# Performance work log

Measured on AMD Instinct MI355X. Metric: run time of the kernel, lower is better.

The kernel has to match this reference:

```python
import jax, jax.numpy as jnp
import numpy as np

N_NODES = 100000


def _gcn_norm(edge_index, num_nodes):
    # add self loops
    src, dst = edge_index[0], edge_index[1]
    loop = jnp.arange(num_nodes, dtype=src.dtype)
    row = jnp.concatenate([src, loop])  # [E+N]
    col = jnp.concatenate([dst, loop])
    ew = jnp.ones(row.shape[0], dtype=jnp.float32)
    deg = jax.ops.segment_sum(ew, col, num_segments=num_nodes)  # [N]
    dinv = jnp.where(deg > 0, jax.lax.rsqrt(deg), 0.0)
    norm = dinv[row] * ew * dinv[col]  # [E+N]
    return row, col, norm


def setup_inputs() -> dict:
    key = jax.random.key(0)
    k1, k2, k3 = jax.random.split(key, 3)
    x = jax.random.normal(k1, (N_NODES, 64), dtype=jnp.float32)
    edge_index = jax.random.randint(k2, (2, 1280000), 0, N_NODES, dtype=jnp.int64)
    W = jax.random.normal(k3, (40, 64), dtype=jnp.float32) * (1.0 / np.sqrt(64))
    b = jnp.zeros((40,), dtype=jnp.float32)
    return {"x": x, "edge_index": edge_index, "W": W, "b": b}


def reference(x, edge_index, W, b):
    K = 3
    row, col, norm = _gcn_norm(edge_index, N_NODES)
    h = x
    for _ in range(K):
        # gather from source nodes, scale by symmetric norm, scatter-add to dst
        msg = norm[:, None] * h[row]  # [E+N, F]
        h = jax.ops.segment_sum(msg, col, num_segments=N_NODES)
    logits = h @ W.T + b  # [N, C]
    return jax.nn.log_softmax(logits, axis=1)
```

## Files before the change

kernel.cpp:

```cpp
#include <hip/hip_runtime.h>

#define F_IN 64
#define F_OUT 40
#define USTRIDE 32
#define UQ4 8
#define QPN 5

#define PART_BLK 256
#define PART_EPB 16
#define PART_TILE (PART_BLK * PART_EPB)
#define BSHIFT 8
#define BCAP 4096
#define MAXB 512

#define WSTRIDE 17
#define NPB 51

__device__ inline unsigned pk2(float x, float y) {
    unsigned a = __float_as_uint(x); a = (a + 0x7FFFu + ((a >> 16) & 1u)) >> 16;
    unsigned b = __float_as_uint(y); b = (b + 0x7FFFu + ((b >> 16) & 1u)) >> 16;
    return a | (b << 16);
}
__device__ inline void up2(unsigned u, float& a, float& b) {
    a = __uint_as_float(u << 16); b = __uint_as_float(u & 0xFFFF0000u);
}

__global__ __launch_bounds__(PART_BLK) void partition_kernel(const int* __restrict__ src,
                                                             const int* __restrict__ dst,
                                                             int* __restrict__ bfill,
                                                             unsigned* __restrict__ staging,
                                                             int E, int nbk) {
    __shared__ int hist[MAXB];
    __shared__ int base[MAXB];
    int tid = threadIdx.x;
    for (int b = tid; b < nbk; b += PART_BLK) hist[b] = 0;
    __syncthreads();

    int rank[PART_EPB];
    int bk[PART_EPB];
    unsigned rec[PART_EPB];
    int eb = blockIdx.x * PART_TILE + tid;
#pragma unroll
    for (int k = 0; k < PART_EPB; ++k) {
        int e = eb + k * PART_BLK;
        if (e < E) {
            int r = src[e];
            int c = dst[e];
            int b = c >> BSHIFT;
            bk[k] = b;
            rec[k] = (unsigned)r | ((unsigned)(c & 255) << 17);
            rank[k] = atomicAdd(&hist[b], 1);
        } else {
            bk[k] = -1;
        }
    }
    __syncthreads();
    for (int b = tid; b < nbk; b += PART_BLK) {
        int h = hist[b];
        base[b] = h ? (b * BCAP + atomicAdd(&bfill[b], h)) : 0;
    }
    __syncthreads();
#pragma unroll
    for (int k = 0; k < PART_EPB; ++k) {
        if (bk[k] >= 0) staging[base[bk[k]] + rank[k]] = rec[k];
    }
}

__global__ __launch_bounds__(256) void bucket_finalize_kernel(const unsigned* __restrict__ staging,
                                                              const int* __restrict__ bfill,
                                                              int* __restrict__ rowptr,
                                                              float* __restrict__ dinv,
                                                              float* __restrict__ dinv2,
                                                              int* __restrict__ srcs, int n, int E) {
    int b = blockIdx.x;
    __shared__ int h[256];
    __shared__ int cur[256];
    __shared__ int sbase;
    int tid = threadIdx.x;
    h[tid] = 0;
    if (tid == 0) sbase = 0;
    __syncthreads();

    int part = 0;
    for (int j = tid; j < b; j += 256) part += bfill[j];
    if (part) atomicAdd(&sbase, part);

    int cnt = bfill[b];
    const unsigned* rec = staging + (size_t)b * BCAP;
    for (int i = tid; i < cnt; i += 256) {
        atomicAdd(&h[rec[i] >> 17], 1);
    }
    __syncthreads();

    int base = sbase;
    int v = h[tid];
    for (int off = 1; off < 256; off <<= 1) {
        int t = (tid >= off) ? h[tid - off] : 0;
        __syncthreads();
        h[tid] += t;
        __syncthreads();
    }
    int excl = h[tid] - v;
    int node = (b << BSHIFT) | tid;
    if (node < n) {
        rowptr[node] = base + excl;
        float r = rsqrtf((float)v + 1.0f);
        dinv[node] = r;
        dinv2[node] = r * r;
    }
    if (b == 0 && tid == 0) rowptr[n] = E;
    cur[tid] = base + excl;
    __syncthreads();

    for (int i = tid; i < cnt; i += 256) {
        unsigned rv = rec[i];
        int pos = atomicAdd(&cur[rv >> 17], 1);
        srcs[pos] = (int)(rv & 0x1FFFFu);
    }
}

__global__ __launch_bounds__(256, 4) void proj_kernel(const float* __restrict__ x,
                                                      const float* __restrict__ W,
                                                      const float* __restrict__ dinv,
                                                      unsigned* __restrict__ u, int n) {
    __shared__ float Ws[F_OUT * WSTRIDE * 4];
    for (int i = threadIdx.x; i < F_OUT * F_IN; i += 256) {
        int c = i >> 6;
        int k = i & 63;
        Ws[c * (WSTRIDE * 4) + k] = W[i];
    }
    __syncthreads();

    int t = blockIdx.x * 256 + threadIdx.x;
    int g = t >> 2;
    int q = t & 3;
    int n0 = 2 * g;
    if (n0 >= n) return;
    int n1 = n0 + 1;

    const float4* xp0 = (const float4*)(x + (size_t)n0 * F_IN);
    const float4* xp1 = (const float4*)(x + (size_t)n1 * F_IN);
    const float4* Wq  = (const float4*)Ws + (size_t)(q * 10) * WSTRIDE;

    float acc0[10], acc1[10];
#pragma unroll
    for (int c = 0; c < 10; ++c) { acc0[c] = 0.0f; acc1[c] = 0.0f; }

#pragma unroll 1
    for (int f4 = 0; f4 < F_IN / 4; ++f4) {
        float4 x0 = xp0[f4];
        float4 x1 = xp1[f4];
#pragma unroll
        for (int c = 0; c < 10; ++c) {
            float4 w = Wq[c * WSTRIDE + f4];
            acc0[c] += x0.x * w.x + x0.y * w.y + x0.z * w.z + x0.w * w.w;
            acc1[c] += x1.x * w.x + x1.y * w.y + x1.z * w.z + x1.w * w.w;
        }
    }

    float d0 = dinv[n0];
    float d1 = dinv[n1];
    unsigned* up0 = u + (size_t)n0 * USTRIDE + q * 5;
    unsigned* up1 = u + (size_t)n1 * USTRIDE + q * 5;
#pragma unroll
    for (int j = 0; j < 5; ++j) {
        up0[j] = pk2(d0 * acc0[2 * j], d0 * acc0[2 * j + 1]);
        up1[j] = pk2(d1 * acc1[2 * j], d1 * acc1[2 * j + 1]);
    }
}

__global__ __launch_bounds__(256) void propagate_kernel(const int* __restrict__ rowptr,
                                                        const int* __restrict__ srcs,
                                                        const float* __restrict__ dinv2,
                                                        const unsigned* __restrict__ ucur,
                                                        unsigned* __restrict__ unew, int n) {
    int t = blockIdx.x * blockDim.x + threadIdx.x;
    int node = t / QPN;
    int q = t - node * QPN;
    if (node >= n) return;

    int beg = rowptr[node];
    int end = rowptr[node + 1];

    const uint4* U = (const uint4*)ucur;
    uint4 sv = U[(size_t)node * UQ4 + q];
    float a0, a1, a2, a3, a4, a5, a6, a7;
    up2(sv.x, a0, a1); up2(sv.y, a2, a3); up2(sv.z, a4, a5); up2(sv.w, a6, a7);

    int i = beg;
    for (; i + 3 < end; i += 4) {
        int s0 = srcs[i], s1 = srcs[i + 1], s2 = srcs[i + 2], s3 = srcs[i + 3];
        uint4 v0 = U[(size_t)s0 * UQ4 + q];
        uint4 v1 = U[(size_t)s1 * UQ4 + q];
        uint4 v2 = U[(size_t)s2 * UQ4 + q];
        uint4 v3 = U[(size_t)s3 * UQ4 + q];
        float b0, b1;
        up2(v0.x, b0, b1); a0 += b0; a1 += b1;
        up2(v0.y, b0, b1); a2 += b0; a3 += b1;
        up2(v0.z, b0, b1); a4 += b0; a5 += b1;
        up2(v0.w, b0, b1); a6 += b0; a7 += b1;
        up2(v1.x, b0, b1); a0 += b0; a1 += b1;
        up2(v1.y, b0, b1); a2 += b0; a3 += b1;
        up2(v1.z, b0, b1); a4 += b0; a5 += b1;
        up2(v1.w, b0, b1); a6 += b0; a7 += b1;
        up2(v2.x, b0, b1); a0 += b0; a1 += b1;
        up2(v2.y, b0, b1); a2 += b0; a3 += b1;
        up2(v2.z, b0, b1); a4 += b0; a5 += b1;
        up2(v2.w, b0, b1); a6 += b0; a7 += b1;
        up2(v3.x, b0, b1); a0 += b0; a1 += b1;
        up2(v3.y, b0, b1); a2 += b0; a3 += b1;
        up2(v3.z, b0, b1); a4 += b0; a5 += b1;
        up2(v3.w, b0, b1); a6 += b0; a7 += b1;
    }
    for (; i < end; ++i) {
        uint4 v = U[(size_t)srcs[i] * UQ4 + q];
        float b0, b1;
        up2(v.x, b0, b1); a0 += b0; a1 += b1;
        up2(v.y, b0, b1); a2 += b0; a3 += b1;
        up2(v.z, b0, b1); a4 += b0; a5 += b1;
        up2(v.w, b0, b1); a6 += b0; a7 += b1;
    }

    float ds = dinv2[node];
    uint4 o;
    o.x = pk2(ds * a0, ds * a1);
    o.y = pk2(ds * a2, ds * a3);
    o.z = pk2(ds * a4, ds * a5);
    o.w = pk2(ds * a6, ds * a7);
    ((uint4*)unew)[(size_t)node * UQ4 + q] = o;
}

__global__ __launch_bounds__(256) void propagate_lsm_kernel(const int* __restrict__ rowptr,
                                                            const int* __restrict__ srcs,
                                                            const float* __restrict__ dinv,
                                                            const unsigned* __restrict__ ucur,
                                                            const float* __restrict__ bias,
                                                            float* __restrict__ out, int n) {
    __shared__ float red[256];
    int tid = threadIdx.x;
    int gl = tid / QPN;
    int q  = tid - gl * QPN;
    int node = blockIdx.x * NPB + gl;
    bool active = (gl < NPB) && (node < n);

    float a0 = 0, a1 = 0, a2 = 0, a3 = 0, a4 = 0, a5 = 0, a6 = 0, a7 = 0;
    float dv = 0.0f;
    if (active) {
        int beg = rowptr[node];
        int end = rowptr[node + 1];
        const uint4* U = (const uint4*)ucur;
        uint4 sv = U[(size_t)node * UQ4 + q];
        up2(sv.x, a0, a1); up2(sv.y, a2, a3); up2(sv.z, a4, a5); up2(sv.w, a6, a7);
        int i = beg;
        for (; i + 3 < end; i += 4) {
            int s0 = srcs[i], s1 = srcs[i + 1], s2 = srcs[i + 2], s3 = srcs[i + 3];
            uint4 v0 = U[(size_t)s0 * UQ4 + q];
            uint4 v1 = U[(size_t)s1 * UQ4 + q];
            uint4 v2 = U[(size_t)s2 * UQ4 + q];
            uint4 v3 = U[(size_t)s3 * UQ4 + q];
            float b0, b1;
            up2(v0.x, b0, b1); a0 += b0; a1 += b1;
            up2(v0.y, b0, b1); a2 += b0; a3 += b1;
            up2(v0.z, b0, b1); a4 += b0; a5 += b1;
            up2(v0.w, b0, b1); a6 += b0; a7 += b1;
            up2(v1.x, b0, b1); a0 += b0; a1 += b1;
            up2(v1.y, b0, b1); a2 += b0; a3 += b1;
            up2(v1.z, b0, b1); a4 += b0; a5 += b1;
            up2(v1.w, b0, b1); a6 += b0; a7 += b1;
            up2(v2.x, b0, b1); a0 += b0; a1 += b1;
            up2(v2.y, b0, b1); a2 += b0; a3 += b1;
            up2(v2.z, b0, b1); a4 += b0; a5 += b1;
            up2(v2.w, b0, b1); a6 += b0; a7 += b1;
            up2(v3.x, b0, b1); a0 += b0; a1 += b1;
            up2(v3.y, b0, b1); a2 += b0; a3 += b1;
            up2(v3.z, b0, b1); a4 += b0; a5 += b1;
            up2(v3.w, b0, b1); a6 += b0; a7 += b1;
        }
        for (; i < end; ++i) {
            uint4 v = U[(size_t)srcs[i] * UQ4 + q];
            float b0, b1;
            up2(v.x, b0, b1); a0 += b0; a1 += b1;
            up2(v.y, b0, b1); a2 += b0; a3 += b1;
            up2(v.z, b0, b1); a4 += b0; a5 += b1;
            up2(v.w, b0, b1); a6 += b0; a7 += b1;
        }
        dv = dinv[node];
    }

    float y0 = dv * a0 + bias[q * 8 + 0];
    float y1 = dv * a1 + bias[q * 8 + 1];
    float y2 = dv * a2 + bias[q * 8 + 2];
    float y3 = dv * a3 + bias[q * 8 + 3];
    float y4 = dv * a4 + bias[q * 8 + 4];
    float y5 = dv * a5 + bias[q * 8 + 5];
    float y6 = dv * a6 + bias[q * 8 + 6];
    float y7 = dv * a7 + bias[q * 8 + 7];

    float pm = fmaxf(fmaxf(fmaxf(y0, y1), fmaxf(y2, y3)),
                     fmaxf(fmaxf(y4, y5), fmaxf(y6, y7)));
    red[tid] = active ? pm : -1e30f;
    __syncthreads();
    int base = tid - q;
    float mx = fmaxf(fmaxf(fmaxf(red[base], red[base + 1]), fmaxf(red[base + 2], red[base + 3])),
                     red[base + 4]);
    __syncthreads();
    float ps = __expf(y0 - mx) + __expf(y1 - mx) + __expf(y2 - mx) + __expf(y3 - mx)
             + __expf(y4 - mx) + __expf(y5 - mx) + __expf(y6 - mx) + __expf(y7 - mx);
    red[tid] = active ? ps : 0.0f;
    __syncthreads();
    float se = red[base] + red[base + 1] + red[base + 2] + red[base + 3] + red[base + 4];
    float lse = mx + __logf(se);

    if (active) {
        float4* p = (float4*)(out + (size_t)node * F_OUT + q * 8);
        float4 o0, o1;
        o0.x = y0 - lse; o0.y = y1 - lse; o0.z = y2 - lse; o0.w = y3 - lse;
        o1.x = y4 - lse; o1.y = y5 - lse; o1.z = y6 - lse; o1.w = y7 - lse;
        p[0] = o0;
        p[1] = o1;
    }
}

extern "C" void kernel_launch(void* const* d_in, const int* in_sizes, int n_in,
                              void* d_out, int out_size, void* d_ws, size_t ws_size,
                              hipStream_t stream) {
    const float* x  = (const float*)d_in[0];
    const int*   ei = (const int*)d_in[1];
    const float* W  = (const float*)d_in[2];
    const float* b  = (const float*)d_in[3];

    const int N = in_sizes[0] / F_IN;
    const int E = in_sizes[1] / 2;
    const int* src = ei;
    const int* dst = ei + E;
    const int nbk = (N + (1 << BSHIFT) - 1) >> BSHIFT;

    char* base = (char*)d_ws;
    size_t off = 0;
    auto alloc = [&](size_t bytes) {
        char* p = base + off;
        off = (off + bytes + 255) & ~(size_t)255;
        return p;
    };
    float*    dinv    = (float*)   alloc((size_t)N * 4);
    float*    dinv2   = (float*)   alloc((size_t)N * 4);
    int*      rowptr  = (int*)     alloc((size_t)(N + 1) * 4);
    int*      bfill   = (int*)     alloc((size_t)MAXB * 4);
    unsigned* staging = (unsigned*)alloc((size_t)nbk * BCAP * 4);
    int*      srcs_s  = (int*)     alloc((size_t)E * 4);
    unsigned* uA      = (unsigned*)alloc((size_t)N * USTRIDE * 4);
    unsigned* uB      = (unsigned*)alloc((size_t)N * USTRIDE * 4);
    float*    outp    = (float*)d_out;

    hipMemsetAsync(bfill, 0, (size_t)nbk * 4, stream);
    partition_kernel<<<(E + PART_TILE - 1) / PART_TILE, PART_BLK, 0, stream>>>(
        src, dst, bfill, staging, E, nbk);

    bucket_finalize_kernel<<<nbk, 256, 0, stream>>>(staging, bfill, rowptr,
                                                    dinv, dinv2, srcs_s, N, E);

    proj_kernel<<<((size_t)N * 2 + 255) / 256, 256, 0, stream>>>(x, W, dinv, uA, N);

    const int pt = N * QPN;
    const int pg = (pt + 255) / 256;
    propagate_kernel<<<pg, 256, 0, stream>>>(rowptr, srcs_s, dinv2, uA, uB, N);
    propagate_kernel<<<pg, 256, 0, stream>>>(rowptr, srcs_s, dinv2, uB, uA, N);

    const int fb = (N + NPB - 1) / NPB;
    propagate_lsm_kernel<<<fb, 256, 0, stream>>>(rowptr, srcs_s, dinv, uA, b, outp, N);
}
```

Measured before the change: 210.3 us.

## Sort nodes by in-degree to balance warp work in propagation kernels

Builds a degree histogram during bucket finalize, scans it, and constructs a permutation of nodes grouped by in-degree. The propagation kernels then process nodes in this permuted order so threads in a wavefront have similar edge counts, which reduces divergence and tail imbalance. This adds two small kernels and an extra indirection through perm, and makes the output writes for each node scattered rather than contiguous.

Result: slower. 232.0 us (+10.3%).

```diff
diff --git a/kernel.cpp b/kernel.cpp
--- a/kernel.cpp
+++ b/kernel.cpp
@@ -15,6 +15,7 @@
 
 #define WSTRIDE 17
 #define NPB 51
+#define NDEG 64
 
 __device__ inline unsigned pk2(float x, float y) {
     unsigned a = __float_as_uint(x); a = (a + 0x7FFFu + ((a >> 16) & 1u)) >> 16;
@@ -68,6 +69,7 @@
 
 __global__ __launch_bounds__(256) void bucket_finalize_kernel(const unsigned* __restrict__ staging,
                                                               const int* __restrict__ bfill,
+                                                              int* __restrict__ dhist,
                                                               int* __restrict__ rowptr,
                                                               float* __restrict__ dinv,
                                                               float* __restrict__ dinv2,
@@ -75,9 +77,11 @@
     int b = blockIdx.x;
     __shared__ int h[256];
     __shared__ int cur[256];
+    __shared__ int ldh[NDEG];
     __shared__ int sbase;
     int tid = threadIdx.x;
     h[tid] = 0;
+    if (tid < NDEG) ldh[tid] = 0;
     if (tid == 0) sbase = 0;
     __syncthreads();
 
@@ -94,14 +98,19 @@
 
     int base = sbase;
     int v = h[tid];
+    int node = (b << BSHIFT) | tid;
+    if (node < n) atomicAdd(&ldh[v < NDEG ? v : NDEG - 1], 1);
     for (int off = 1; off < 256; off <<= 1) {
         int t = (tid >= off) ? h[tid - off] : 0;
         __syncthreads();
         h[tid] += t;
         __syncthreads();
     }
+    if (tid < NDEG) {
+        int c = ldh[tid];
+        if (c) atomicAdd(&dhist[tid], c);
+    }
     int excl = h[tid] - v;
-    int node = (b << BSHIFT) | tid;
     if (node < n) {
         rowptr[node] = base + excl;
         float r = rsqrtf((float)v + 1.0f);
@@ -117,6 +126,46 @@
         int pos = atomicAdd(&cur[rv >> 17], 1);
         srcs[pos] = (int)(rv & 0x1FFFFu);
     }
+}
+
+__global__ __launch_bounds__(64) void dscan_kernel(const int* __restrict__ dhist,
+                                                   int* __restrict__ dcur) {
+    __shared__ int s[NDEG];
+    int tid = threadIdx.x;
+    int v = dhist[tid];
+    s[tid] = v;
+    __syncthreads();
+    for (int off = 1; off < NDEG; off <<= 1) {
+        int t = (tid >= off) ? s[tid - off] : 0;
+        __syncthreads();
+        s[tid] += t;
+        __syncthreads();
+    }
+    dcur[tid] = s[tid] - v;
+}
+
+__global__ __launch_bounds__(256) void perm_build_kernel(const int* __restrict__ rowptr,
+                                                         int* __restrict__ dcur,
+                                                         int* __restrict__ perm, int n) {
+    __shared__ int lh[NDEG];
+    __shared__ int lbase[NDEG];
+    int tid = threadIdx.x;
+    if (tid < NDEG) lh[tid] = 0;
+    __syncthreads();
+    int node = blockIdx.x * 256 + tid;
+    int d = 0, rank = 0;
+    if (node < n) {
+        int deg = rowptr[node + 1] - rowptr[node];
+        d = deg < NDEG ? deg : NDEG - 1;
+        rank = atomicAdd(&lh[d], 1);
+    }
+    __syncthreads();
+    if (tid < NDEG) {
+        int c = lh[tid];
+        lbase[tid] = c ? atomicAdd(&dcur[tid], c) : 0;
+    }
+    __syncthreads();
+    if (node < n) perm[lbase[d] + rank] = node;
 }
 
 __global__ __launch_bounds__(256, 4) void proj_kernel(const float* __restrict__ x,
@@ -171,13 +220,15 @@
 
 __global__ __launch_bounds__(256) void propagate_kernel(const int* __restrict__ rowptr,
                                                         const int* __restrict__ srcs,
+                                                        const int* __restrict__ perm,
                                                         const float* __restrict__ dinv2,
                                                         const unsigned* __restrict__ ucur,
                                                         unsigned* __restrict__ unew, int n) {
     int t = blockIdx.x * blockDim.x + threadIdx.x;
-    int node = t / QPN;
-    int q = t - node * QPN;
-    if (node >= n) return;
+    int g = t / QPN;
+    int q = t - g * QPN;
+    if (g >= n) return;
+    int node = perm[g];
 
     int beg = rowptr[node];
     int end = rowptr[node + 1];
@@ -232,6 +283,7 @@
 
 __global__ __launch_bounds__(256) void propagate_lsm_kernel(const int* __restrict__ rowptr,
                                                             const int* __restrict__ srcs,
+                                                            const int* __restrict__ perm,
                                                             const float* __restrict__ dinv,
                                                             const unsigned* __restrict__ ucur,
                                                             const float* __restrict__ bias,
@@ -240,8 +292,9 @@
     int tid = threadIdx.x;
     int gl = tid / QPN;
     int q  = tid - gl * QPN;
-    int node = blockIdx.x * NPB + gl;
-    bool active = (gl < NPB) && (node < n);
+    int g = blockIdx.x * NPB + gl;
+    bool active = (gl < NPB) && (g < n);
+    int node = active ? perm[g] : 0;
 
     float a0 = 0, a1 = 0, a2 = 0, a3 = 0, a4 = 0, a5 = 0, a6 = 0, a7 = 0;
     float dv = 0.0f;
@@ -345,27 +398,34 @@
     float*    dinv    = (float*)   alloc((size_t)N * 4);
     float*    dinv2   = (float*)   alloc((size_t)N * 4);
     int*      rowptr  = (int*)     alloc((size_t)(N + 1) * 4);
-    int*      bfill   = (int*)     alloc((size_t)MAXB * 4);
+    int*      meta    = (int*)     alloc((size_t)(MAXB + 2 * NDEG) * 4);
+    int*      bfill   = meta;
+    int*      dhist   = meta + MAXB;
+    int*      dcur    = meta + MAXB + NDEG;
+    int*      perm    = (int*)     alloc((size_t)N * 4);
     unsigned* staging = (unsigned*)alloc((size_t)nbk * BCAP * 4);
     int*      srcs_s  = (int*)     alloc((size_t)E * 4);
     unsigned* uA      = (unsigned*)alloc((size_t)N * USTRIDE * 4);
     unsigned* uB      = (unsigned*)alloc((size_t)N * USTRIDE * 4);
     float*    outp    = (float*)d_out;
 
-    hipMemsetAsync(bfill, 0, (size_t)nbk * 4, stream);
+    hipMemsetAsync(meta, 0, (size_t)(MAXB + 2 * NDEG) * 4, stream);
     partition_kernel<<<(E + PART_TILE - 1) / PART_TILE, PART_BLK, 0, stream>>>(
         src, dst, bfill, staging, E, nbk);
 
-    bucket_finalize_kernel<<<nbk, 256, 0, stream>>>(staging, bfill, rowptr,
+    bucket_finalize_kernel<<<nbk, 256, 0, stream>>>(staging, bfill, dhist, rowptr,
                                                     dinv, dinv2, srcs_s, N, E);
 
     proj_kernel<<<((size_t)N * 2 + 255) / 256, 256, 0, stream>>>(x, W, dinv, uA, N);
+
+    dscan_kernel<<<1, 64, 0, stream>>>(dhist, dcur);
+    perm_build_kernel<<<(N + 255) / 256, 256, 0, stream>>>(rowptr, dcur, perm, N);
 
     const int pt = N * QPN;
     const int pg = (pt + 255) / 256;
-    propagate_kernel<<<pg, 256, 0, stream>>>(rowptr, srcs_s, dinv2, uA, uB, N);
-    propagate_kernel<<<pg, 256, 0, stream>>>(rowptr, srcs_s, dinv2, uB, uA, N);
+    propagate_kernel<<<pg, 256, 0, stream>>>(rowptr, srcs_s, perm, dinv2, uA, uB, N);
+    propagate_kernel<<<pg, 256, 0, stream>>>(rowptr, srcs_s, perm, dinv2, uB, uA, N);
 
     const int fb = (N + NPB - 1) / NPB;
-    propagate_lsm_kernel<<<fb, 256, 0, stream>>>(rowptr, srcs_s, dinv, uA, b, outp, N);
-}
+    propagate_lsm_kernel<<<fb, 256, 0, stream>>>(rowptr, srcs_s, perm, dinv, uA, b, outp, N);
+}
```
